# Optimization experiments

Hardware: AMD Instinct MI355X
Metric: run time of the kernel (lower is better)

Reference implementation:

```python
import jax, jax.numpy as jnp
import numpy as np
from jax import lax

B, DIM, H, W = 8, 128, 64, 64
CQ, DI, DS, RK = 32, 64, 16, 2  # quarter dim, d_inner=2*CQ, d_state, dt_rank=ceil(32/16)
EPS = 1e-5


def _dw(x, w, dil):
    # depthwise conv, x: [B,C,H,W], w: [C,1,kh,kw], torch padding='same'
    return lax.conv_general_dilated(x, w, (1, 1), 'SAME', rhs_dilation=(dil, dil),
                                    dimension_numbers=('NCHW', 'OIHW', 'NCHW'),
                                    feature_group_count=x.shape[1])


def _ln(x, g, b):
    mu = jnp.mean(x, -1, keepdims=True)
    v = jnp.mean((x - mu) ** 2, -1, keepdims=True)
    return (x - mu) * lax.rsqrt(v + EPS) * g + b


def _bn_eval(x, g, b):
    # BatchNorm2d eval mode with default running stats (mean 0, var 1)
    return x * lax.rsqrt(jnp.float32(1.0) + EPS) * g[None, :, None, None] + b[None, :, None, None]


def _axial_dw(x, kh, kw, k3, g, b, dil):
    y = _dw(x, kw, dil)   # (1,w) mixer
    y = _dw(y, kh, dil)   # (h,1) mixer
    y = _dw(y, k3, dil)   # 3x3 dw
    return _bn_eval(y, g, b) + x


def _vss(x, ln_g, ln_b, in_w, conv_w, conv_b, xproj_w, dtw, dtb, A_logs, Ds, on_g, on_b, out_w):
    # x: [B,H,W,CQ] channels-last; VMamba VSSBlock: x + SS2D(LN(x))
    Bb, Hh, Ww, _ = x.shape
    L = Hh * Ww
    xz = _ln(x, ln_g, ln_b) @ in_w.T                      # [B,H,W,2*DI]
    xw, z = jnp.split(xz, 2, axis=-1)
    xc = jax.nn.silu(_dw(xw.transpose(0, 3, 1, 2), conv_w, 1) + conv_b[None, :, None, None])
    xf = xc.reshape(Bb, DI, L)                            # row-major scan
    xwh = xc.transpose(0, 1, 3, 2).reshape(Bb, DI, L)     # column-major scan
    xs = jnp.stack([xf, xwh, jnp.flip(xf, -1), jnp.flip(xwh, -1)], axis=1)  # [B,4,DI,L]
    x_dbl = jnp.einsum('bkdl,kcd->bkcl', xs, xproj_w)     # [B,4,RK+2*DS,L]
    delta = jax.nn.softplus(jnp.einsum('bkrl,kdr->bkdl', x_dbl[:, :, :RK], dtw) + dtb[None, :, :, None])
    Bs, Cs = x_dbl[:, :, RK:RK + DS], x_dbl[:, :, RK + DS:]
    A = -jnp.exp(A_logs)                                  # [4,DI,DS]

    def step(h, t):
        u, d, Bt, Ct = t                                  # u,d:[B,4,DI]; Bt,Ct:[B,4,DS]
        h = h * jnp.exp(d[..., None] * A) + (d * u)[..., None] * Bt[:, :, None, :]
        return h, jnp.einsum('bkdn,bkn->bkd', h, Ct)

    seq = (xs.transpose(3, 0, 1, 2), delta.transpose(3, 0, 1, 2),
           Bs.transpose(3, 0, 1, 2), Cs.transpose(3, 0, 1, 2))
    _, ys = lax.scan(step, jnp.zeros((Bb, 4, DI, DS), x.dtype), seq)  # [L,B,4,DI]
    ys = ys.transpose(1, 2, 3, 0) + Ds[None, :, :, None] * xs         # [B,4,DI,L]
    y = ys[:, 0] + jnp.flip(ys[:, 2], -1)
    y_wh = ys[:, 1] + jnp.flip(ys[:, 3], -1)
    y = y + y_wh.reshape(Bb, DI, Ww, Hh).transpose(0, 1, 3, 2).reshape(Bb, DI, L)
    y = _ln(y.reshape(Bb, DI, Hh, Ww).transpose(0, 2, 3, 1), on_g, on_b)
    return x + (y * jax.nn.silu(z)) @ out_w.T


def _forward(x, dw1_kh, dw1_kw, dw1_k3, dw1_g, dw1_b, dw2_kh, dw2_kw, dw2_k3, dw2_g, dw2_b,
             dw3_kh, dw3_kw, dw3_k3, dw3_g, dw3_b, ln_g, ln_b, in_w, conv_w, conv_b, xproj_w,
             dtw, dtb, A_logs, Ds, on_g, on_b, out_w, scale1, scale2, scale3, scale4, bn_g, bn_b):
    x1, x2, x3, x4 = jnp.split(x, 4, axis=1)
    vp = (ln_g, ln_b, in_w, conv_w, conv_b, xproj_w, dtw, dtb, A_logs, Ds, on_g, on_b, out_w)

    def branch(xi, kh, kw, k3, g, b, dil, s):
        y = _axial_dw(xi, kh, kw, k3, g, b, dil)
        y = _vss(y.transpose(0, 2, 3, 1), *vp).transpose(0, 3, 1, 2)
        return y * s

    y1 = branch(x1, dw1_kh, dw1_kw, dw1_k3, dw1_g, dw1_b, 1, scale1)
    y2 = branch(x2, dw2_kh, dw2_kw, dw2_k3, dw2_g, dw2_b, 2, scale2)
    y3 = branch(x3, dw3_kh, dw3_kw, dw3_k3, dw3_g, dw3_b, 3, scale3)
    y4 = x4 * scale4
    return jax.nn.relu(_bn_eval(jnp.concatenate([y1, y2, y3, y4], 1), bn_g, bn_b))


def setup_inputs():
    ks = jax.random.split(jax.random.key(0), 40)
    rn = lambda k, s, sc: jax.random.normal(k, s, jnp.float32) * sc
    inp = {'x': jax.random.normal(ks[0], (B, DIM, H, W), jnp.float32)}
    for i, n in enumerate(['dw1', 'dw2', 'dw3']):
        inp[n + '_kh'] = rn(ks[1 + 3 * i], (CQ, 1, 7, 1), 0.2)
        inp[n + '_kw'] = rn(ks[2 + 3 * i], (CQ, 1, 1, 7), 0.2)
        inp[n + '_k3'] = rn(ks[3 + 3 * i], (CQ, 1, 3, 3), 0.2)
        inp[n + '_g'] = jnp.ones((CQ,))
        inp[n + '_b'] = jnp.zeros((CQ,))
    inp['ln_g'] = jnp.ones((CQ,))
    inp['ln_b'] = jnp.zeros((CQ,))
    inp['in_w'] = rn(ks[10], (2 * DI, CQ), 0.1)
    inp['conv_w'] = rn(ks[11], (DI, 1, 3, 3), 0.2)
    inp['conv_b'] = jnp.zeros((DI,))
    inp['xproj_w'] = rn(ks[12], (4, RK + 2 * DS, DI), 0.1)
    inp['dtw'] = rn(ks[13], (4, DI, RK), 0.5)
    inp['dtb'] = rn(ks[14], (4, DI), 0.5)
    inp['A_logs'] = jnp.log(jnp.broadcast_to(jnp.arange(1, DS + 1, dtype=jnp.float32), (4, DI, DS)))
    inp['Ds'] = jnp.ones((4, DI))
    inp['on_g'] = jnp.ones((DI,))
    inp['on_b'] = jnp.zeros((DI,))
    inp['out_w'] = rn(ks[15], (CQ, DI), 0.1)
    for n in ['scale1', 'scale2', 'scale3', 'scale4']:
        inp[n] = jnp.ones((1,))
    inp['bn_g'] = jnp.ones((DIM,))
    inp['bn_b'] = jnp.zeros((DIM,))
    return inp


def reference(x, dw1_kh, dw1_kw, dw1_k3, dw1_g, dw1_b, dw2_kh, dw2_kw, dw2_k3, dw2_g, dw2_b,
              dw3_kh, dw3_kw, dw3_k3, dw3_g, dw3_b, ln_g, ln_b, in_w, conv_w, conv_b, xproj_w,
              dtw, dtb, A_logs, Ds, on_g, on_b, out_w, scale1, scale2, scale3, scale4, bn_g, bn_b):
    return _forward(x, dw1_kh, dw1_kw, dw1_k3, dw1_g, dw1_b, dw2_kh, dw2_kw, dw2_k3, dw2_g, dw2_b,
                    dw3_kh, dw3_kw, dw3_k3, dw3_g, dw3_b, ln_g, ln_b, in_w, conv_w, conv_b, xproj_w,
                    dtw, dtb, A_logs, Ds, on_g, on_b, out_w, scale1, scale2, scale3, scale4, bn_g, bn_b)
```

## Files before the change

### kernel.cpp

```cpp
#include <hip/hip_runtime.h>
#include <hip/hip_bf16.h>
#include <cstdint>

typedef unsigned short ushort_t;
typedef float f32x2 __attribute__((ext_vector_type(2)));

__device__ __forceinline__ float softplus2(float x){
    return fmaxf(x, 0.f) + __logf(1.f + __expf(-fabsf(x)));
}
__device__ __forceinline__ float siluf(float x){
    return x / (1.f + __expf(-x));
}
__device__ __forceinline__ float b2f(ushort_t u){
    union { uint32_t i; float f; } v; v.i = ((uint32_t)u)<<16; return v.f;
}
__device__ __forceinline__ ushort_t f2b(float f){
    uint32_t x = __float_as_uint(f);
    uint32_t r = (x + 0x7FFFu + ((x>>16)&1u)) >> 16;
    return (ushort_t)r;
}
__device__ __forceinline__ f32x2 m2(f32x2 v, float s){ f32x2 r; r.x=v.x*s; r.y=v.y*s; return r; }

struct AxialParams {
    const float* kh[3]; const float* kw[3]; const float* k3[3];
    const float* g[3];  const float* b[3];
};

__global__ __launch_bounds__(256) void k_axial(const float* __restrict__ x,
                                               float* __restrict__ Y0, AxialParams P){
    __shared__ float s0[4096];
    __shared__ float s1[4096];
    int bid = blockIdx.x;
    int i = bid >> 8;
    int rem = bid & 255;
    int b = rem >> 5, c = rem & 31;
    int dil = i + 1;
    const float* xin = x + ((size_t)(b*128 + i*32 + c))*4096;
    float wkw[7], wkh[7], wk3[9];
    #pragma unroll
    for(int t=0;t<7;t++){ wkw[t]=P.kw[i][c*7+t]; wkh[t]=P.kh[i][c*7+t]; }
    #pragma unroll
    for(int t=0;t<9;t++) wk3[t]=P.k3[i][c*9+t];
    float gc = P.g[i][c], bc = P.b[i][c];
    int tid = threadIdx.x;
    for(int idx=tid; idx<4096; idx+=256) s0[idx]=xin[idx];
    __syncthreads();
    for(int idx=tid; idx<4096; idx+=256){
        int h=idx>>6, w=idx&63; float a=0.f;
        #pragma unroll
        for(int t=0;t<7;t++){ int ww=w+(t-3)*dil; if(ww>=0&&ww<64) a=fmaf(s0[h*64+ww],wkw[t],a); }
        s1[idx]=a;
    }
    __syncthreads();
    for(int idx=tid; idx<4096; idx+=256){
        int h=idx>>6, w=idx&63; float a=0.f;
        #pragma unroll
        for(int t=0;t<7;t++){ int hh=h+(t-3)*dil; if(hh>=0&&hh<64) a=fmaf(s1[hh*64+w],wkh[t],a); }
        s0[idx]=a;
    }
    __syncthreads();
    const float inv = rsqrtf(1.00001f);
    float* out = Y0 + ((size_t)(i*8+b)*32 + c)*4096;
    for(int idx=tid; idx<4096; idx+=256){
        int h=idx>>6, w=idx&63; float a=0.f;
        #pragma unroll
        for(int t=0;t<9;t++){
            int hh=h+((t/3)-1)*dil, ww=w+((t%3)-1)*dil;
            if(hh>=0&&hh<64&&ww>=0&&ww<64) a=fmaf(s0[hh*64+ww],wk3[t],a);
        }
        out[idx] = a*inv*gc + bc + xin[idx];
    }
}

__global__ __launch_bounds__(256) void k_lnproj(const float* __restrict__ Y0,
        const float* __restrict__ ln_g, const float* __restrict__ ln_b,
        const float* __restrict__ in_w, ushort_t* __restrict__ XW, ushort_t* __restrict__ ZS){
    __shared__ float W[128*32];
    int tid=threadIdx.x;
    for(int idx=tid; idx<1024; idx+=256)
        *reinterpret_cast<float4*>(&W[idx*4]) = *reinterpret_cast<const float4*>(&in_w[idx*4]);
    __syncthreads();
    int pg = blockIdx.x*256 + tid;
    int ib = pg>>12, p = pg&4095;
    const float* src = Y0 + (size_t)ib*32*4096;
    float t[32];
    float mu=0.f;
    #pragma unroll
    for(int c=0;c<32;c++){ t[c]=src[c*4096+p]; mu+=t[c]; }
    mu *= (1.f/32.f);
    float v=0.f;
    #pragma unroll
    for(int c=0;c<32;c++){ float d=t[c]-mu; v+=d*d; }
    v *= (1.f/32.f);
    float rs = rsqrtf(v+1e-5f);
    #pragma unroll
    for(int c=0;c<32;c++) t[c] = (t[c]-mu)*rs*ln_g[c] + ln_b[c];
    ushort_t* xw = XW + (size_t)ib*64*4096 + p;
    ushort_t* zs = ZS + (size_t)ib*64*4096 + p;
    for(int j=0;j<64;j++){
        float wv[32], wv2[32];
        const float4* wp  = reinterpret_cast<const float4*>(&W[j*32]);
        const float4* wp2 = reinterpret_cast<const float4*>(&W[(j+64)*32]);
        #pragma unroll
        for(int q=0;q<8;q++){
            *reinterpret_cast<float4*>(&wv[q*4])  = wp[q];
            *reinterpret_cast<float4*>(&wv2[q*4]) = wp2[q];
        }
        float a=0.f, a2=0.f;
        #pragma unroll
        for(int c=0;c<32;c++){
            a  = fmaf(t[c], wv[c],  a);
            a2 = fmaf(t[c], wv2[c], a2);
        }
        xw[(size_t)j*4096] = f2b(a);
        zs[(size_t)j*4096] = f2b(siluf(a2));
    }
}

__global__ __launch_bounds__(256) void k_dwt(const ushort_t* __restrict__ XW,
        const float* __restrict__ cw, const float* __restrict__ cb,
        ushort_t* __restrict__ XC, ushort_t* __restrict__ XCT){
    __shared__ ushort_t sin_[4096];
    __shared__ ushort_t tr[64*66];
    int bid=blockIdx.x, tid=threadIdx.x;
    int d = bid&63;
    const ushort_t* src = XW + (size_t)bid*4096;
    for(int idx=tid; idx<1024; idx+=256)
        *reinterpret_cast<ushort4*>(&sin_[idx*4]) = *reinterpret_cast<const ushort4*>(&src[idx*4]);
    float wk[9];
    #pragma unroll
    for(int t=0;t<9;t++) wk[t]=cw[d*9+t];
    float bias=cb[d];
    __syncthreads();
    ushort_t* outp = XC + (size_t)bid*4096;
    for(int idx=tid; idx<4096; idx+=256){
        int h=idx>>6, wq=idx&63;
        float a=bias;
        #pragma unroll
        for(int t=0;t<9;t++){
            int hh=h+(t/3)-1, ww=wq+(t%3)-1;
            if(hh>=0&&hh<64&&ww>=0&&ww<64) a=fmaf(b2f(sin_[hh*64+ww]),wk[t],a);
        }
        ushort_t vb = f2b(siluf(a));
        outp[idx]=vb;
        tr[wq*66+h]=vb;
    }
    __syncthreads();
    ushort_t* outt = XCT + (size_t)bid*4096;
    for(int idx=tid; idx<4096; idx+=256){
        outt[idx]=tr[(idx>>6)*66+(idx&63)];
    }
}

__global__ __launch_bounds__(128) void k_xdbl(const ushort_t* __restrict__ XC, const ushort_t* __restrict__ XCT,
        const float* __restrict__ xproj, ushort_t* __restrict__ XBb, ushort_t* __restrict__ XCc,
        float* __restrict__ DT){
    __shared__ ushort_t tile[64][128];
    __shared__ float Wt[64][36];
    int bid=blockIdx.x, tid=threadIdx.x;
    int lb = bid&31, t=(bid>>5)&1, ib=bid>>6;
    int m0 = lb*128;
    const ushort_t* src = (t?XCT:XC) + (size_t)ib*64*4096;
    for(int idx=tid; idx<2048; idx+=128){
        int dd=idx>>5, q=(idx&31)*4;
        *reinterpret_cast<ushort4*>(&tile[dd][q]) =
            *reinterpret_cast<const ushort4*>(&src[(size_t)dd*4096 + m0 + q]);
    }
    int m = m0 + tid;
    for(int pass=0; pass<2; ++pass){
        int k = t + 2*pass;
        __syncthreads();
        for(int idx=tid; idx<2176; idx+=128){
            int c=idx>>6, dd=idx&63;
            Wt[dd][c]=xproj[k*2176+idx];
        }
        __syncthreads();
        float acc[34];
        #pragma unroll
        for(int c=0;c<34;c++) acc[c]=0.f;
        for(int dd=0;dd<64;dd++){
            float u = b2f(tile[dd][tid]);
            float wv[36];
            const float4* wp = reinterpret_cast<const float4*>(&Wt[dd][0]);
            *reinterpret_cast<float4*>(&wv[0])  = wp[0];
            *reinterpret_cast<float4*>(&wv[4])  = wp[1];
            *reinterpret_cast<float4*>(&wv[8])  = wp[2];
            *reinterpret_cast<float4*>(&wv[12]) = wp[3];
            *reinterpret_cast<float4*>(&wv[16]) = wp[4];
            *reinterpret_cast<float4*>(&wv[20]) = wp[5];
            *reinterpret_cast<float4*>(&wv[24]) = wp[6];
            *reinterpret_cast<float4*>(&wv[28]) = wp[7];
            *reinterpret_cast<float2*>(&wv[32]) = *reinterpret_cast<const float2*>(&Wt[dd][32]);
            #pragma unroll
            for(int c=0;c<34;c++) acc[c] = fmaf(u, wv[c], acc[c]);
        }
        int l = pass ? (4095-m) : m;
        DT[((size_t)(ib*4+k)*2)*4096 + l]   = acc[0];
        DT[((size_t)(ib*4+k)*2+1)*4096 + l] = acc[1];
        ushort_t* ob = XBb + ((size_t)(ib*4+k)*16)*4096 + l;
        ushort_t* oc = XCc + ((size_t)(ib*4+k)*16)*4096 + l;
        #pragma unroll
        for(int c=0;c<16;c++){
            ob[(size_t)c*4096]=f2b(acc[2+c]);
            oc[(size_t)c*4096]=f2b(acc[18+c]);
        }
    }
}

__device__ __forceinline__ int chunk_swz(int c0){
    int xcd = c0 & 7, grp = c0 >> 3;
    return (grp >> 1)*16 + xcd*2 + (grp & 1);
}

template<bool UNI>
__device__ __forceinline__ void scan1_body(int w,int d,float dt0,float dt1,float db,
    const float* An, f32x2* h2, float& S,
    const float (*sB)[32][16], const float (*sdt)[32][2], const ushort_t (*su)[66])
{
    for(int t=0;t<32;t++){
        const float* dp=&sdt[w][t][0];
        float delta=softplus2(fmaf(dt0,dp[0],fmaf(dt1,dp[1],db)));
        S+=delta;
        int j = w? 31-t : t;
        float du = delta*b2f(su[j][d]);
        float bb[16];
        const float4* bp=reinterpret_cast<const float4*>(&sB[w][t][0]);
        reinterpret_cast<float4*>(bb)[0]=bp[0];
        reinterpret_cast<float4*>(bb)[1]=bp[1];
        reinterpret_cast<float4*>(bb)[2]=bp[2];
        reinterpret_cast<float4*>(bb)[3]=bp[3];
        if(UNI){
            float r1=__expf(delta*An[0]);
            float r2=r1*r1, r4=r2*r2, r8=r4*r4;
            f32x2 a0={r1,r2};
            f32x2 aa1=m2(a0,r2), aa2=m2(a0,r4), aa3=m2(aa1,r4);
            f32x2 aa4=m2(a0,r8), aa5=m2(aa1,r8), aa6=m2(aa2,r8), aa7=m2(aa3,r8);
            f32x2 du2={du,du};
            const f32x2* b2p=reinterpret_cast<const f32x2*>(bb);
            h2[0]=h2[0]*a0 +du2*b2p[0];
            h2[1]=h2[1]*aa1+du2*b2p[1];
            h2[2]=h2[2]*aa2+du2*b2p[2];
            h2[3]=h2[3]*aa3+du2*b2p[3];
            h2[4]=h2[4]*aa4+du2*b2p[4];
            h2[5]=h2[5]*aa5+du2*b2p[5];
            h2[6]=h2[6]*aa6+du2*b2p[6];
            h2[7]=h2[7]*aa7+du2*b2p[7];
        } else {
            float* hf=reinterpret_cast<float*>(h2);
            #pragma unroll
            for(int n=0;n<16;n++){ float a=__expf(delta*An[n]); hf[n]=fmaf(hf[n],a,du*bb[n]); }
        }
    }
}

__global__ __launch_bounds__(128) void k_scan1(const ushort_t* __restrict__ XBb, const float* __restrict__ DT,
        const ushort_t* __restrict__ XC, const ushort_t* __restrict__ XCT,
        const float* __restrict__ dtw, const float* __restrict__ dtb,
        const float* __restrict__ A_logs,
        ushort_t* __restrict__ CHS, float* __restrict__ SD){
    __shared__ float sB[2][32][16];
    __shared__ float sdt[2][32][2];
    __shared__ ushort_t su[32][66];
    int bid=blockIdx.x, tid=threadIdx.x;
    int ib = bid>>8; int rem = bid&255; int p = rem>>7; int ch = chunk_swz(rem&127);
    int w = tid>>6, d = tid&63;
    int l0 = ch*32, r0 = 4064 - l0;
    const ushort_t* B0 = XBb + (size_t)(4*ib+p)*16*4096;
    const ushort_t* B1 = XBb + (size_t)(4*ib+p+2)*16*4096;
    for(int idx=tid; idx<256; idx+=128){
        int n=idx&15, qi=(idx>>4)&7, w2=idx>>7;
        int base=(w2? r0 : l0) + qi*4;
        ushort4 v = *reinterpret_cast<const ushort4*>(&(w2?B1:B0)[(size_t)n*4096 + base]);
        int sl=qi*4;
        sB[w2][sl+0][n]=b2f(v.x); sB[w2][sl+1][n]=b2f(v.y);
        sB[w2][sl+2][n]=b2f(v.z); sB[w2][sl+3][n]=b2f(v.w);
    }
    {
        const float* D0 = DT + (size_t)(4*ib+p)*2*4096;
        const float* D1 = DT + (size_t)(4*ib+p+2)*2*4096;
        int w2=tid>>6; int rem2=tid&63; int s=rem2>>1; int r=rem2&1;
        sdt[w2][s][r]      = (w2? D1 : D0)[(size_t)r*4096 + (w2? r0 : l0) + s];
        sdt[w2][s+16][r]   = (w2? D1 : D0)[(size_t)r*4096 + (w2? r0 : l0) + s + 16];
    }
    const ushort_t* U = (p?XCT:XC) + (size_t)ib*64*4096;
    for(int idx=tid; idx<512; idx+=128){
        int r=idx>>3, q=(idx&7)*4;
        ushort4 v = *reinterpret_cast<const ushort4*>(&U[(size_t)r*4096 + l0 + q]);
        su[q+0][r]=v.x; su[q+1][r]=v.y; su[q+2][r]=v.z; su[q+3][r]=v.w;
    }
    __syncthreads();
    int k = p + 2*w;
    float dt0=dtw[(k*64+d)*2], dt1=dtw[(k*64+d)*2+1], db=dtb[k*64+d];
    float An[16];
    #pragma unroll
    for(int n=0;n<16;n++) An[n] = -__expf(A_logs[(k*64+d)*16+n]);
    bool st = true;
    #pragma unroll
    for(int n=1;n<16;n++) st = st && (fabsf(An[n]-(n+1)*An[0]) <= 1e-4f*fabsf(An[n]) + 1e-6f);
    bool uni = (bool)__all((int)st);
    f32x2 h2[8];
    #pragma unroll
    for(int i=0;i<8;i++){ h2[i].x=0.f; h2[i].y=0.f; }
    float S=0.f;
    if(uni) scan1_body<true >(w,d,dt0,dt1,db,An,h2,S,sB,sdt,su);
    else    scan1_body<false>(w,d,dt0,dt1,db,An,h2,S,sB,sdt,su);
    int chd = w ? 127-ch : ch;
    ushort_t* o = CHS + ((size_t)(4*ib+k)*128 + chd)*1024 + d*16;
    const float* hf = reinterpret_cast<const float*>(h2);
    #pragma unroll
    for(int n=0;n<16;n++) o[n]=f2b(hf[n]);
    SD[((size_t)(4*ib+k)*128 + chd)*64 + d]=S;
}

__global__ __launch_bounds__(256) void k_scan2(const float* __restrict__ A_logs,
        const float* __restrict__ SD, ushort_t* __restrict__ CHS){
    __shared__ float sS[2048];
    int g=blockIdx.x; int ibk=g>>2; int dg=g&3; int tid=threadIdx.x;
    for(int idx=tid; idx<2048; idx+=256){
        int c=idx>>4, dl=idx&15;
        sS[idx]=SD[((size_t)ibk*128+c)*64 + dg*16 + dl];
    }
    __syncthreads();
    int dl=tid>>4, n=tid&15, k=ibk&3;
    int d=dg*16+dl;
    float An = -__expf(A_logs[(k*64+d)*16+n]);
    float H=0.f;
    for(int c=0;c<128;c++){
        float pc = __expf(An*sS[c*16+dl]);
        size_t o = ((size_t)ibk*128+c)*1024 + dg*256 + tid;
        float loc = b2f(CHS[o]);
        CHS[o]=f2b(H);
        H = fmaf(H, pc, loc);
    }
}

template<bool UNI, bool ADD>
__device__ __forceinline__ void scan3_phase(int w,int d,float dt0,float dt1,float db,
    const float* An, f32x2* h2, int T0,
    const float (*sB)[32][16], const float (*sC)[32][16],
    const float (*sdt)[32][2], const ushort_t (*su)[66], ushort_t (*sy)[66])
{
    for(int tt=0;tt<16;tt++){
        int t = T0 + tt;
        const float* dp=&sdt[w][t][0];
        float delta=softplus2(fmaf(dt0,dp[0],fmaf(dt1,dp[1],db)));
        int j = w? 31-t : t;
        float du = delta*b2f(su[j][d]);
        float bb[16], cc[16];
        const float4* bp=reinterpret_cast<const float4*>(&sB[w][t][0]);
        const float4* cp=reinterpret_cast<const float4*>(&sC[w][t][0]);
        reinterpret_cast<float4*>(bb)[0]=bp[0]; reinterpret_cast<float4*>(bb)[1]=bp[1];
        reinterpret_cast<float4*>(bb)[2]=bp[2]; reinterpret_cast<float4*>(bb)[3]=bp[3];
        reinterpret_cast<float4*>(cc)[0]=cp[0]; reinterpret_cast<float4*>(cc)[1]=cp[1];
        reinterpret_cast<float4*>(cc)[2]=cp[2]; reinterpret_cast<float4*>(cc)[3]=cp[3];
        float y;
        if(UNI){
            float r1=__expf(delta*An[0]);
            float r2=r1*r1, r4=r2*r2, r8=r4*r4;
            f32x2 a0={r1,r2};
            f32x2 aa1=m2(a0,r2), aa2=m2(a0,r4), aa3=m2(aa1,r4);
            f32x2 aa4=m2(a0,r8), aa5=m2(aa1,r8), aa6=m2(aa2,r8), aa7=m2(aa3,r8);
            f32x2 du2={du,du};
            f32x2 y2={0.f,0.f};
            const f32x2* b2p=reinterpret_cast<const f32x2*>(bb);
            const f32x2* c2p=reinterpret_cast<const f32x2*>(cc);
            h2[0]=h2[0]*a0 +du2*b2p[0]; y2=y2+h2[0]*c2p[0];
            h2[1]=h2[1]*aa1+du2*b2p[1]; y2=y2+h2[1]*c2p[1];
            h2[2]=h2[2]*aa2+du2*b2p[2]; y2=y2+h2[2]*c2p[2];
            h2[3]=h2[3]*aa3+du2*b2p[3]; y2=y2+h2[3]*c2p[3];
            h2[4]=h2[4]*aa4+du2*b2p[4]; y2=y2+h2[4]*c2p[4];
            h2[5]=h2[5]*aa5+du2*b2p[5]; y2=y2+h2[5]*c2p[5];
            h2[6]=h2[6]*aa6+du2*b2p[6]; y2=y2+h2[6]*c2p[6];
            h2[7]=h2[7]*aa7+du2*b2p[7]; y2=y2+h2[7]*c2p[7];
            y = y2.x + y2.y;
        } else {
            y=0.f;
            float* hf=reinterpret_cast<float*>(h2);
            #pragma unroll
            for(int n=0;n<16;n++){
                float a=__expf(delta*An[n]);
                hf[n]=fmaf(hf[n],a,du*bb[n]);
                y=fmaf(hf[n],cc[n],y);
            }
        }
        if(ADD) sy[j][d]=f2b(b2f(sy[j][d])+y);
        else    sy[j][d]=f2b(y);
    }
}

__global__ __launch_bounds__(128) void k_scan3(const ushort_t* __restrict__ XBb, const ushort_t* __restrict__ XCc,
        const float* __restrict__ DT,
        const ushort_t* __restrict__ XC, const ushort_t* __restrict__ XCT,
        const float* __restrict__ dtw, const float* __restrict__ dtb,
        const float* __restrict__ A_logs,
        const ushort_t* __restrict__ CHS,
        ushort_t* __restrict__ YS){
    __shared__ float sB[2][32][16];
    __shared__ float sC[2][32][16];
    __shared__ float sdt[2][32][2];
    __shared__ ushort_t su[32][66];
    __shared__ ushort_t sy[32][66];
    int bid=blockIdx.x, tid=threadIdx.x;
    int ib = bid>>8; int rem = bid&255; int p = rem>>7; int ch = chunk_swz(rem&127);
    int w = tid>>6, d = tid&63;
    int l0 = ch*32, r0 = 4064 - l0;
    const ushort_t* B0 = XBb + (size_t)(4*ib+p)*16*4096;
    const ushort_t* B1 = XBb + (size_t)(4*ib+p+2)*16*4096;
    const ushort_t* C0 = XCc + (size_t)(4*ib+p)*16*4096;
    const ushort_t* C1 = XCc + (size_t)(4*ib+p+2)*16*4096;
    for(int idx=tid; idx<512; idx+=128){
        int n=idx&15, qi=(idx>>4)&7, w2=(idx>>7)&1, arr=idx>>8;
        int base=(w2? r0 : l0) + qi*4;
        const ushort_t* S = arr? (w2?C1:C0) : (w2?B1:B0);
        ushort4 v = *reinterpret_cast<const ushort4*>(&S[(size_t)n*4096 + base]);
        float (*dst)[32][16] = arr? sC : sB;
        int sl=qi*4;
        dst[w2][sl+0][n]=b2f(v.x); dst[w2][sl+1][n]=b2f(v.y);
        dst[w2][sl+2][n]=b2f(v.z); dst[w2][sl+3][n]=b2f(v.w);
    }
    {
        const float* D0 = DT + (size_t)(4*ib+p)*2*4096;
        const float* D1 = DT + (size_t)(4*ib+p+2)*2*4096;
        int w2=tid>>6; int rem2=tid&63; int s=rem2>>1; int r=rem2&1;
        sdt[w2][s][r]      = (w2? D1 : D0)[(size_t)r*4096 + (w2? r0 : l0) + s];
        sdt[w2][s+16][r]   = (w2? D1 : D0)[(size_t)r*4096 + (w2? r0 : l0) + s + 16];
    }
    const ushort_t* U = (p?XCT:XC) + (size_t)ib*64*4096;
    for(int idx=tid; idx<512; idx+=128){
        int r=idx>>3, q=(idx&7)*4;
        ushort4 v = *reinterpret_cast<const ushort4*>(&U[(size_t)r*4096 + l0 + q]);
        su[q+0][r]=v.x; su[q+1][r]=v.y; su[q+2][r]=v.z; su[q+3][r]=v.w;
    }
    __syncthreads();
    int k = p + 2*w;
    float dt0=dtw[(k*64+d)*2], dt1=dtw[(k*64+d)*2+1], db=dtb[k*64+d];
    float An[16];
    #pragma unroll
    for(int n=0;n<16;n++) An[n] = -__expf(A_logs[(k*64+d)*16+n]);
    bool st = true;
    #pragma unroll
    for(int n=1;n<16;n++) st = st && (fabsf(An[n]-(n+1)*An[0]) <= 1e-4f*fabsf(An[n]) + 1e-6f);
    bool uni = (bool)__all((int)st);
    int chd = w ? 127-ch : ch;
    const ushort_t* e = CHS + ((size_t)(4*ib+k)*128 + chd)*1024 + d*16;
    f32x2 h2[8];
    {
        float* hf = reinterpret_cast<float*>(h2);
        #pragma unroll
        for(int n=0;n<16;n++) hf[n]=b2f(e[n]);
    }
    if(uni) scan3_phase<true ,false>(w,d,dt0,dt1,db,An,h2, 0,sB,sC,sdt,su,sy);
    else    scan3_phase<false,false>(w,d,dt0,dt1,db,An,h2, 0,sB,sC,sdt,su,sy);
    __syncthreads();
    if(uni) scan3_phase<true ,true >(w,d,dt0,dt1,db,An,h2,16,sB,sC,sdt,su,sy);
    else    scan3_phase<false,true >(w,d,dt0,dt1,db,An,h2,16,sB,sC,sdt,su,sy);
    __syncthreads();
    ushort_t* plane = YS + (size_t)(ib*2+p)*262144;
    if(p==0){
        for(int idx=tid; idx<512; idx+=128){
            int jr=idx>>4, q=(idx&15)*4;
            ushort4 v;
            v.x=sy[jr][q+0]; v.y=sy[jr][q+1]; v.z=sy[jr][q+2]; v.w=sy[jr][q+3];
            *reinterpret_cast<ushort4*>(&plane[(size_t)(l0+jr)*64 + q]) = v;
        }
    } else {
        int hi = l0>>6, lo0 = l0&63;
        for(int idx=tid; idx<512; idx+=128){
            int jr=idx>>4, q=(idx&15)*4;
            ushort4 v;
            v.x=sy[jr][q+0]; v.y=sy[jr][q+1]; v.z=sy[jr][q+2]; v.w=sy[jr][q+3];
            *reinterpret_cast<ushort4*>(&plane[(size_t)(lo0+jr)*4096 + hi*64 + q]) = v;
        }
    }
}

__global__ __launch_bounds__(256) void k_final2(const ushort_t* __restrict__ YS,
        const ushort_t* __restrict__ ZS, const float* __restrict__ Y0,
        const ushort_t* __restrict__ XC, const float* __restrict__ Ds,
        const float* __restrict__ on_g, const float* __restrict__ on_b,
        const float* __restrict__ out_w,
        const float* __restrict__ s1, const float* __restrict__ s2, const float* __restrict__ s3,
        const float* __restrict__ bn_g, const float* __restrict__ bn_b,
        float* __restrict__ out){
    __shared__ float W[32*64];
    __shared__ float sD[64];
    int tid=threadIdx.x;
    for(int idx=tid; idx<512; idx+=256)
        *reinterpret_cast<float4*>(&W[idx*4]) = *reinterpret_cast<const float4*>(&out_w[idx*4]);
    if(tid<64) sD[tid]=Ds[tid]+Ds[64+tid]+Ds[128+tid]+Ds[192+tid];
    __syncthreads();
    int pg=blockIdx.x*256+tid;
    int ib=pg>>12, p=pg&4095;
    int i=ib>>3, b=ib&7;
    const ushort_t* r0p = YS + (size_t)(ib*2+0)*262144 + (size_t)p*64;
    const ushort_t* r1p = YS + (size_t)(ib*2+1)*262144 + (size_t)p*64;
    const ushort_t* xc = XC + (size_t)ib*64*4096 + p;
    float y[64];
    float mu=0.f;
    #pragma unroll
    for(int qq=0; qq<8; ++qq){
        ushort4 a0 = reinterpret_cast<const ushort4*>(r0p)[qq*2];
        ushort4 b0 = reinterpret_cast<const ushort4*>(r0p)[qq*2+1];
        ushort4 a1 = reinterpret_cast<const ushort4*>(r1p)[qq*2];
        ushort4 b1 = reinterpret_cast<const ushort4*>(r1p)[qq*2+1];
        const ushort_t* u0=reinterpret_cast<const ushort_t*>(&a0);
        const ushort_t* u1=reinterpret_cast<const ushort_t*>(&b0);
        const ushort_t* v0=reinterpret_cast<const ushort_t*>(&a1);
        const ushort_t* v1=reinterpret_cast<const ushort_t*>(&b1);
        #pragma unroll
        for(int e=0;e<4;e++){
            int dd=qq*8+e;
            y[dd]   = b2f(u0[e])+b2f(v0[e]) + sD[dd]  *b2f(xc[(size_t)dd*4096]);
            y[dd+4] = b2f(u1[e])+b2f(v1[e]) + sD[dd+4]*b2f(xc[(size_t)(dd+4)*4096]);
            mu += y[dd]+y[dd+4];
        }
    }
    mu*=(1.f/64.f);
    float v=0.f;
    #pragma unroll
    for(int dd=0;dd<64;dd++){ float q=y[dd]-mu; v+=q*q; }
    v*=(1.f/64.f);
    float rs=rsqrtf(v+1e-5f);
    const ushort_t* zs = ZS + (size_t)ib*64*4096 + p;
    #pragma unroll
    for(int dd=0;dd<64;dd++){
        float yn=(y[dd]-mu)*rs*on_g[dd]+on_b[dd];
        y[dd]=yn*b2f(zs[(size_t)dd*4096]);
    }
    float sc = (i==0)?s1[0]:((i==1)?s2[0]:s3[0]);
    const float inv = rsqrtf(1.00001f);
    const float* y0 = Y0 + (size_t)ib*32*4096 + p;
    for(int c=0;c<32;c++){
        float wv[64];
        const float4* wp = reinterpret_cast<const float4*>(&W[c*64]);
        #pragma unroll
        for(int q=0;q<16;q++) *reinterpret_cast<float4*>(&wv[q*4]) = wp[q];
        float a=0.f;
        #pragma unroll
        for(int dd=0;dd<64;dd++) a=fmaf(y[dd],wv[dd],a);
        float o=(y0[(size_t)c*4096]+a)*sc;
        int chn=i*32+c;
        float vv=fmaf(o*inv, bn_g[chn], bn_b[chn]);
        out[((size_t)b*128+chn)*4096 + p]=fmaxf(vv,0.f);
    }
}

__global__ __launch_bounds__(256) void k_branch4(const float* __restrict__ x,
        const float* __restrict__ s4, const float* __restrict__ bn_g,
        const float* __restrict__ bn_b, float* __restrict__ out){
    int g=blockIdx.x*256+threadIdx.x;
    int b=g>>17; int rem=g&131071; int c=rem>>12; int p=rem&4095;
    int chn=96+c;
    const float inv=rsqrtf(1.00001f);
    float v=x[((size_t)b*128+chn)*4096+p]*s4[0];
    v=fmaf(v*inv, bn_g[chn], bn_b[chn]);
    out[((size_t)b*128+chn)*4096+p]=fmaxf(v,0.f);
}

extern "C" void kernel_launch(void* const* d_in, const int* in_sizes, int n_in,
                              void* d_out, int out_size, void* d_ws, size_t ws_size,
                              hipStream_t stream) {
    const float* x      = (const float*)d_in[0];
    const float* ln_g   = (const float*)d_in[16];
    const float* ln_b   = (const float*)d_in[17];
    const float* in_w   = (const float*)d_in[18];
    const float* conv_w = (const float*)d_in[19];
    const float* conv_b = (const float*)d_in[20];
    const float* xproj  = (const float*)d_in[21];
    const float* dtw    = (const float*)d_in[22];
    const float* dtb    = (const float*)d_in[23];
    const float* A_logs = (const float*)d_in[24];
    const float* Ds     = (const float*)d_in[25];
    const float* on_g   = (const float*)d_in[26];
    const float* on_b   = (const float*)d_in[27];
    const float* out_w  = (const float*)d_in[28];
    const float* sc1    = (const float*)d_in[29];
    const float* sc2    = (const float*)d_in[30];
    const float* sc3    = (const float*)d_in[31];
    const float* sc4    = (const float*)d_in[32];
    const float* bn_g   = (const float*)d_in[33];
    const float* bn_b   = (const float*)d_in[34];

    AxialParams P;
    for(int i=0;i<3;i++){
        P.kh[i]=(const float*)d_in[1+5*i];
        P.kw[i]=(const float*)d_in[2+5*i];
        P.k3[i]=(const float*)d_in[3+5*i];
        P.g[i] =(const float*)d_in[4+5*i];
        P.b[i] =(const float*)d_in[5+5*i];
    }

    char* base = (char*)d_ws;
    float*    Y0   = (float*)   (base + 0);
    ushort_t* ZS   = (ushort_t*)(base + 12582912);
    ushort_t* XC   = (ushort_t*)(base + 25165824);
    ushort_t* XCT  = (ushort_t*)(base + 37748736);
    ushort_t* XBb  = (ushort_t*)(base + 50331648);
    ushort_t* XW   = (ushort_t*)(base + 50331648);
    ushort_t* XCc  = (ushort_t*)(base + 62914560);
    float*    DT   = (float*)   (base + 75497472);
    ushort_t* CHS  = (ushort_t*)(base + 78643200);
    float*    SD   = (float*)   (base + 103809024);
    ushort_t* YS   = (ushort_t*)(base + 106954752);

    float* out = (float*)d_out;

    k_axial    <<<768,   256, 0, stream>>>(x, Y0, P);
    k_lnproj   <<<384,   256, 0, stream>>>(Y0, ln_g, ln_b, in_w, XW, ZS);
    k_dwt      <<<1536,  256, 0, stream>>>(XW, conv_w, conv_b, XC, XCT);
    k_xdbl     <<<1536,  128, 0, stream>>>(XC, XCT, xproj, XBb, XCc, DT);
    k_scan1    <<<6144,  128, 0, stream>>>(XBb, DT, XC, XCT, dtw, dtb, A_logs, CHS, SD);
    k_scan2    <<<384,   256, 0, stream>>>(A_logs, SD, CHS);
    k_scan3    <<<6144,  128, 0, stream>>>(XBb, XCc, DT, XC, XCT, dtw, dtb, A_logs, CHS, YS);
    k_final2   <<<384,   256, 0, stream>>>(YS, ZS, Y0, XC, Ds, on_g, on_b, out_w,
                                           sc1, sc2, sc3, bn_g, bn_b, out);
    k_branch4  <<<4096,  256, 0, stream>>>(x, sc4, bn_g, bn_b, out);
}
```

Before: 301.3 us.

## Hold xdbl inputs and scan3 outputs in registers, drop LDS tiling and phase sync

k_xdbl now loads each thread's 64-channel input column straight into registers and preloads both directions' projection weights into LDS once. It then computes each output as a separate 64-long dot product, replacing the staged input tile and the per-pass weight reload. k_scan3 merges its two half-scan phases into one unrolled 32-step loop: the forward warp keeps its outputs in registers, the reverse warp writes to LDS, and after one barrier the forward warp sums the two and stores to global. Both kernels get launch_bounds min-blocks hints; the cost is much higher register pressure (64 floats of inputs, 32 y values) and narrower, less vectorised global stores.

```diff
diff --git a/kernel.cpp b/kernel.cpp
--- a/kernel.cpp
+++ b/kernel.cpp
@@ -152,58 +152,52 @@
     }
 }
 
-__global__ __launch_bounds__(128) void k_xdbl(const ushort_t* __restrict__ XC, const ushort_t* __restrict__ XCT,
+__device__ __forceinline__ float dot64(const float* u, const float* Wrow){
+    float acc=0.f;
+    #pragma unroll
+    for(int q=0;q<4;q++){
+        float wv[16];
+        const float4* wp = reinterpret_cast<const float4*>(Wrow + q*16);
+        *reinterpret_cast<float4*>(&wv[0])  = wp[0];
+        *reinterpret_cast<float4*>(&wv[4])  = wp[1];
+        *reinterpret_cast<float4*>(&wv[8])  = wp[2];
+        *reinterpret_cast<float4*>(&wv[12]) = wp[3];
+        #pragma unroll
+        for(int e=0;e<16;e++) acc = fmaf(u[q*16+e], wv[e], acc);
+    }
+    return acc;
+}
+
+__global__ __launch_bounds__(128,4) void k_xdbl(const ushort_t* __restrict__ XC, const ushort_t* __restrict__ XCT,
         const float* __restrict__ xproj, ushort_t* __restrict__ XBb, ushort_t* __restrict__ XCc,
         float* __restrict__ DT){
-    __shared__ ushort_t tile[64][128];
-    __shared__ float Wt[64][36];
+    __shared__ float W2[2][34*64];
     int bid=blockIdx.x, tid=threadIdx.x;
     int lb = bid&31, t=(bid>>5)&1, ib=bid>>6;
-    int m0 = lb*128;
+    int m = lb*128 + tid;
+    for(int idx=tid; idx<2176; idx+=128){
+        W2[0][idx]=xproj[t*2176+idx];
+        W2[1][idx]=xproj[(t+2)*2176+idx];
+    }
     const ushort_t* src = (t?XCT:XC) + (size_t)ib*64*4096;
-    for(int idx=tid; idx<2048; idx+=128){
-        int dd=idx>>5, q=(idx&31)*4;
-        *reinterpret_cast<ushort4*>(&tile[dd][q]) =
-            *reinterpret_cast<const ushort4*>(&src[(size_t)dd*4096 + m0 + q]);
-    }
-    int m = m0 + tid;
+    float u[64];
+    #pragma unroll
+    for(int dd=0; dd<64; dd++) u[dd] = b2f(src[(size_t)dd*4096 + m]);
+    __syncthreads();
+    #pragma unroll
     for(int pass=0; pass<2; ++pass){
         int k = t + 2*pass;
-        __syncthreads();
-        for(int idx=tid; idx<2176; idx+=128){
-            int c=idx>>6, dd=idx&63;
-            Wt[dd][c]=xproj[k*2176+idx];
-        }
-        __syncthreads();
-        float acc[34];
-        #pragma unroll
-        for(int c=0;c<34;c++) acc[c]=0.f;
-        for(int dd=0;dd<64;dd++){
-            float u = b2f(tile[dd][tid]);
-            float wv[36];
-            const float4* wp = reinterpret_cast<const float4*>(&Wt[dd][0]);
-            *reinterpret_cast<float4*>(&wv[0])  = wp[0];
-            *reinterpret_cast<float4*>(&wv[4])  = wp[1];
-            *reinterpret_cast<float4*>(&wv[8])  = wp[2];
-            *reinterpret_cast<float4*>(&wv[12]) = wp[3];
-            *reinterpret_cast<float4*>(&wv[16]) = wp[4];
-            *reinterpret_cast<float4*>(&wv[20]) = wp[5];
-            *reinterpret_cast<float4*>(&wv[24]) = wp[6];
-            *reinterpret_cast<float4*>(&wv[28]) = wp[7];
-            *reinterpret_cast<float2*>(&wv[32]) = *reinterpret_cast<const float2*>(&Wt[dd][32]);
-            #pragma unroll
-            for(int c=0;c<34;c++) acc[c] = fmaf(u, wv[c], acc[c]);
-        }
+        const float* W = &W2[pass][0];
         int l = pass ? (4095-m) : m;
-        DT[((size_t)(ib*4+k)*2)*4096 + l]   = acc[0];
-        DT[((size_t)(ib*4+k)*2+1)*4096 + l] = acc[1];
+        float* dtp = DT + ((size_t)(ib*4+k)*2)*4096 + l;
         ushort_t* ob = XBb + ((size_t)(ib*4+k)*16)*4096 + l;
         ushort_t* oc = XCc + ((size_t)(ib*4+k)*16)*4096 + l;
-        #pragma unroll
-        for(int c=0;c<16;c++){
-            ob[(size_t)c*4096]=f2b(acc[2+c]);
-            oc[(size_t)c*4096]=f2b(acc[18+c]);
-        }
+        dtp[0]    = dot64(u, W);
+        dtp[4096] = dot64(u, W+64);
+        #pragma unroll 4
+        for(int c=0;c<16;c++) ob[(size_t)c*4096]=f2b(dot64(u, W+(2+c)*64));
+        #pragma unroll 4
+        for(int c=0;c<16;c++) oc[(size_t)c*4096]=f2b(dot64(u, W+(18+c)*64));
     }
 }
 
@@ -334,14 +328,14 @@
     }
 }
 
-template<bool UNI, bool ADD>
-__device__ __forceinline__ void scan3_phase(int w,int d,float dt0,float dt1,float db,
-    const float* An, f32x2* h2, int T0,
+template<bool UNI>
+__device__ __forceinline__ void scan3_run(int w,int d,float dt0,float dt1,float db,
+    const float* An, f32x2* h2, float* yreg,
     const float (*sB)[32][16], const float (*sC)[32][16],
     const float (*sdt)[32][2], const ushort_t (*su)[66], ushort_t (*sy)[66])
 {
-    for(int tt=0;tt<16;tt++){
-        int t = T0 + tt;
+    #pragma unroll
+    for(int t=0;t<32;t++){
         const float* dp=&sdt[w][t][0];
         float delta=softplus2(fmaf(dt0,dp[0],fmaf(dt1,dp[1],db)));
         int j = w? 31-t : t;
@@ -383,12 +377,12 @@
                 y=fmaf(hf[n],cc[n],y);
             }
         }
-        if(ADD) sy[j][d]=f2b(b2f(sy[j][d])+y);
-        else    sy[j][d]=f2b(y);
-    }
-}
-
-__global__ __launch_bounds__(128) void k_scan3(const ushort_t* __restrict__ XBb, const ushort_t* __restrict__ XCc,
+        if(w==0) yreg[t]=y;
+        else     sy[j][d]=f2b(y);
+    }
+}
+
+__global__ __launch_bounds__(128,4) void k_scan3(const ushort_t* __restrict__ XBb, const ushort_t* __restrict__ XCc,
         const float* __restrict__ DT,
         const ushort_t* __restrict__ XC, const ushort_t* __restrict__ XCT,
         const float* __restrict__ dtw, const float* __restrict__ dtb,
@@ -449,27 +443,21 @@
         #pragma unroll
         for(int n=0;n<16;n++) hf[n]=b2f(e[n]);
     }
-    if(uni) scan3_phase<true ,false>(w,d,dt0,dt1,db,An,h2, 0,sB,sC,sdt,su,sy);
-    else    scan3_phase<false,false>(w,d,dt0,dt1,db,An,h2, 0,sB,sC,sdt,su,sy);
-    __syncthreads();
-    if(uni) scan3_phase<true ,true >(w,d,dt0,dt1,db,An,h2,16,sB,sC,sdt,su,sy);
-    else    scan3_phase<false,true >(w,d,dt0,dt1,db,An,h2,16,sB,sC,sdt,su,sy);
-    __syncthreads();
-    ushort_t* plane = YS + (size_t)(ib*2+p)*262144;
-    if(p==0){
-        for(int idx=tid; idx<512; idx+=128){
-            int jr=idx>>4, q=(idx&15)*4;
-            ushort4 v;
-            v.x=sy[jr][q+0]; v.y=sy[jr][q+1]; v.z=sy[jr][q+2]; v.w=sy[jr][q+3];
-            *reinterpret_cast<ushort4*>(&plane[(size_t)(l0+jr)*64 + q]) = v;
-        }
-    } else {
-        int hi = l0>>6, lo0 = l0&63;
-        for(int idx=tid; idx<512; idx+=128){
-            int jr=idx>>4, q=(idx&15)*4;
-            ushort4 v;
-            v.x=sy[jr][q+0]; v.y=sy[jr][q+1]; v.z=sy[jr][q+2]; v.w=sy[jr][q+3];
-            *reinterpret_cast<ushort4*>(&plane[(size_t)(lo0+jr)*4096 + hi*64 + q]) = v;
+    float yreg[32];
+    if(uni) scan3_run<true >(w,d,dt0,dt1,db,An,h2,yreg,sB,sC,sdt,su,sy);
+    else    scan3_run<false>(w,d,dt0,dt1,db,An,h2,yreg,sB,sC,sdt,su,sy);
+    __syncthreads();
+    if(w==0){
+        ushort_t* plane = YS + (size_t)(ib*2+p)*262144;
+        if(p==0){
+            #pragma unroll
+            for(int j=0;j<32;j++)
+                plane[(size_t)(l0+j)*64 + d] = f2b(yreg[j] + b2f(sy[j][d]));
+        } else {
+            int hi = l0>>6, lo0 = l0&63;
+            #pragma unroll
+            for(int j=0;j<32;j++)
+                plane[(size_t)(lo0+j)*4096 + hi*64 + d] = f2b(yreg[j] + b2f(sy[j][d]));
         }
     }
 }
```

New measurement: 522.6 us. 73.5% more time.
